# Performance work log

Measured on AMD Instinct MI355X. Metric: run time of the kernel, lower is better.

## Reference

```python
import jax, jax.numpy as jnp
import numpy as np

N, D, H = 8192, 256, 128
KEEP_RATIO = 0.5
TEMP = 1.0
COS_EPS = 1e-4  # torch CosineSimilarity eps
NEG = -9e15


def setup_inputs() -> dict:
    key = jax.random.key(0)
    k1, k2, k3, k4 = jax.random.split(key, 4)
    features = jax.random.normal(k1, (N, D), dtype=jnp.float32)
    adj = jax.random.randint(k2, (N, N), 0, 2, dtype=jnp.int32)
    # module init: Linear weights ~ N(0, 0.001)
    Wq = jax.random.normal(k3, (H, D), dtype=jnp.float32) * 0.001
    Wk = jax.random.normal(k4, (H, D), dtype=jnp.float32) * 0.001
    return {"features": features, "adj": adj, "Wq": Wq, "Wk": Wk}


def _cos_normalize(x):
    # torch cosine: x / max(||x||, eps)
    n = jnp.linalg.norm(x, axis=-1, keepdims=True)
    return x / jnp.maximum(n, COS_EPS)


def reference(features, adj, Wq, Wk):
    # projections [N, H]
    Qn = _cos_normalize(features @ Wq.T)
    Kn = _cos_normalize(features @ Wk.T)
    # raw_att[i, j] = cos(Wq f_j, Wk f_i)  -> [N, N]
    raw_att = Kn @ Qn.T
    att = jnp.where(adj > 0, raw_att, NEG) * TEMP
    att = jax.nn.softmax(att, axis=1)
    prop_fea = att @ features  # [N, D]
    # nodes with no neighbors keep their own features
    adj_mask = (jnp.sum(adj, axis=1) > 0).astype(features.dtype)[:, None]
    prop_fea = adj_mask * prop_fea + (1.0 - adj_mask) * features
    # gate=None branch: fixed keep_ratio mixing
    return (1.0 - KEEP_RATIO) * prop_fea + KEEP_RATIO * features
```

## Files before the change

### kernel.cpp

```cpp
#include <hip/hip_runtime.h>
#include <stdint.h>
#include <stddef.h>

#define NN 8192
#define DD 256
#define HH 128

typedef short bf16x8  __attribute__((ext_vector_type(8)));
typedef float f32x4   __attribute__((ext_vector_type(4)));
typedef float f32x16  __attribute__((ext_vector_type(16)));
typedef int   i32x4   __attribute__((ext_vector_type(4)));

static __device__ __forceinline__ short f2bf(float x){
  unsigned u = __float_as_uint(x);
  u = (u + 0x7FFFu + ((u >> 16) & 1u)) >> 16;
  return (short)(unsigned short)u;
}
static __device__ __forceinline__ bf16x8 cvt8(const float* p){
  f32x4 a = *(const f32x4*)p;
  f32x4 b = *(const f32x4*)(p + 4);
  bf16x8 o;
  o[0]=f2bf(a[0]); o[1]=f2bf(a[1]); o[2]=f2bf(a[2]); o[3]=f2bf(a[3]);
  o[4]=f2bf(b[0]); o[5]=f2bf(b[1]); o[6]=f2bf(b[2]); o[7]=f2bf(b[3]);
  return o;
}
static __device__ __forceinline__ bf16x8 ld16(const void* p){
  i32x4 v = *(const i32x4*)p;
  return __builtin_bit_cast(bf16x8, v);
}

__global__ __launch_bounds__(256) void k_ftfrag(const float* __restrict__ f,
                                                unsigned short* __restrict__ ftf){
  int t = threadIdx.x;
  int fr = blockIdx.x * 4 + (t >> 6);
  int l  = t & 63;
  int jt = fr >> 3, dt = fr & 7;
  int j = jt * 16 + (l >> 5) * 8, d = dt * 32 + (l & 31);
  bf16x8 o;
  #pragma unroll
  for (int e = 0; e < 8; ++e) o[e] = f2bf(f[(size_t)(j + e) * DD + d]);
  *(bf16x8*)(ftf + (size_t)fr * 512 + l * 8) = o;
}

__global__ __launch_bounds__(256) void k_proj(const float* __restrict__ f,
                                              const float* __restrict__ Wq,
                                              const float* __restrict__ Wk,
                                              unsigned short* __restrict__ Qnf,
                                              unsigned short* __restrict__ Kn){
  int t = threadIdx.x, wave = t >> 6, l = t & 63;
  int i0 = blockIdx.x * 64 + wave * 16;
  int lr = l & 15, lk = l >> 4;
  bf16x8 ka[8];
  #pragma unroll
  for (int ks = 0; ks < 8; ++ks)
    ka[ks] = cvt8(f + (size_t)(i0 + lr) * DD + ks * 32 + lk * 8);
  for (int pj = 0; pj < 2; ++pj){
    const float* W = pj ? Wk : Wq;
    f32x4 acc[8];
    #pragma unroll
    for (int n = 0; n < 8; ++n) acc[n] = (f32x4){0.f,0.f,0.f,0.f};
    for (int ks = 0; ks < 8; ++ks)
      #pragma unroll
      for (int n = 0; n < 8; ++n){
        bf16x8 bb = cvt8(W + (size_t)(n * 16 + lr) * DD + ks * 32 + lk * 8);
        acc[n] = __builtin_amdgcn_mfma_f32_16x16x32_bf16(ka[ks], bb, acc[n], 0, 0, 0);
      }
    #pragma unroll
    for (int r = 0; r < 4; ++r){
      float n2 = 0.f;
      #pragma unroll
      for (int n = 0; n < 8; ++n){ float v = acc[n][r]; n2 += v * v; }
      n2 += __shfl_xor(n2, 1); n2 += __shfl_xor(n2, 2);
      n2 += __shfl_xor(n2, 4); n2 += __shfl_xor(n2, 8);
      float s = 1.f / fmaxf(sqrtf(n2), 1e-4f);
      int row = i0 + lk * 4 + r;
      #pragma unroll
      for (int n = 0; n < 8; ++n){
        short v = f2bf(acc[n][r] * s);
        if (pj){
          Kn[(size_t)row * HH + n * 16 + lr] = (unsigned short)v;
        } else {
          size_t off = ((size_t)(row >> 5) * 8 + n) * 512
                     + ((row & 31) + 32 * (lr >> 3)) * 8 + (lr & 7);
          Qnf[off] = (unsigned short)v;
        }
      }
    }
  }
}

__global__ __launch_bounds__(256, 2) void k_attn(
      const int* __restrict__ adj,
      const unsigned short* __restrict__ Qnf, const unsigned short* __restrict__ Kn,
      const unsigned short* __restrict__ ftf,
      float* __restrict__ num_p, float* __restrict__ den_p){
  __shared__ __attribute__((aligned(16))) char p_lds[8192];
  __shared__ __attribute__((aligned(16))) int adj_lds[2][64][64];
  int t = threadIdx.x, wave = t >> 6, l = t & 63;
  int lc = l & 31, h = l >> 5;
  int ig = wave >> 1, jg = wave & 1, wq = wave;
  int ib = blockIdx.x >> 2, js = blockIdx.x & 3;
  int i0 = ib * 64;
  int jbase = js * 2048;

  bf16x8 kb[8];
  { const unsigned short* kp = Kn + (size_t)(i0 + ig * 32 + lc) * HH + h * 8;
    #pragma unroll
    for (int hs = 0; hs < 8; ++hs) kb[hs] = ld16(kp + hs * 16); }

  f32x16 pv00, pv01, pv10, pv11;
  #pragma unroll
  for (int e = 0; e < 16; ++e){ pv00[e]=0.f; pv01[e]=0.f; pv10[e]=0.f; pv11[e]=0.f; }
  float dacc[16];
  #pragma unroll
  for (int r = 0; r < 16; ++r) dacc[r] = 0.f;

  int arow = wave * 16 + (l >> 4);
  int acol = (l & 15) * 4;

  #pragma unroll
  for (int k4 = 0; k4 < 4; ++k4){
    i32x4 v = __builtin_nontemporal_load(
        (const i32x4*)(adj + (size_t)(i0 + arow + k4 * 4) * NN + jbase + acol));
    *(i32x4*)&adj_lds[0][arow + k4 * 4][acol] = v;
  }
  __syncthreads();

  for (int s = 0; s < 32; ++s){
    int j0 = jbase + s * 64;
    int cur = s & 1, nxt = cur ^ 1;

    bf16x8 qv[8];
    { const unsigned short* qb = Qnf + ((size_t)((j0 + jg * 32) >> 5) * 8) * 512 + (size_t)l * 8;
      #pragma unroll
      for (int hs = 0; hs < 8; ++hs) qv[hs] = ld16(qb + hs * 512); }

    i32x4 av[4];
    if (s < 31){
      #pragma unroll
      for (int k4 = 0; k4 < 4; ++k4)
        av[k4] = __builtin_nontemporal_load(
            (const i32x4*)(adj + (size_t)(i0 + arow + k4 * 4) * NN + j0 + 64 + acol));
    }

    bf16x8 bv[8];
    { const unsigned short* fb = ftf + ((size_t)(j0 >> 4) * 8 + wq * 2) * 512 + (size_t)l * 8;
      #pragma unroll
      for (int ks = 0; ks < 4; ++ks){
        bv[ks * 2]     = ld16(fb + ks * 4096);
        bv[ks * 2 + 1] = ld16(fb + ks * 4096 + 512); } }

    f32x16 st;
    #pragma unroll
    for (int e = 0; e < 16; ++e) st[e] = 0.f;
    #pragma unroll
    for (int hs = 0; hs < 8; ++hs)
      st = __builtin_amdgcn_mfma_f32_32x32x16_bf16(kb[hs], qv[hs], st, 0, 0, 0);

    #pragma unroll
    for (int r = 0; r < 16; ++r){
      int row = ig * 32 + (r & 3) + 8 * (r >> 2) + 4 * h;
      int a = adj_lds[cur][row][jg * 32 + lc];
      float wv = (a > 0) ? __expf(st[r]) : 0.f;
      dacc[r] += wv;
      int byo = row * 128 + (((jg * 32 + lc) * 2) ^ ((row & 7) << 4));
      *(unsigned short*)(p_lds + byo) = (unsigned short)f2bf(wv);
    }
    __syncthreads();

    if (s < 31){
      #pragma unroll
      for (int k4 = 0; k4 < 4; ++k4)
        *(i32x4*)&adj_lds[nxt][arow + k4 * 4][acol] = av[k4];
    }

    #pragma unroll
    for (int ks = 0; ks < 4; ++ks){
      int ko = (ks * 32 + h * 16) ^ ((lc & 7) << 4);
      bf16x8 pa0 = ld16(p_lds + lc * 128 + ko);
      bf16x8 pa1 = ld16(p_lds + (32 + lc) * 128 + ko);
      pv00 = __builtin_amdgcn_mfma_f32_32x32x16_bf16(pa0, bv[ks*2],   pv00, 0,0,0);
      pv01 = __builtin_amdgcn_mfma_f32_32x32x16_bf16(pa0, bv[ks*2+1], pv01, 0,0,0);
      pv10 = __builtin_amdgcn_mfma_f32_32x32x16_bf16(pa1, bv[ks*2],   pv10, 0,0,0);
      pv11 = __builtin_amdgcn_mfma_f32_32x32x16_bf16(pa1, bv[ks*2+1], pv11, 0,0,0);
    }
    __syncthreads();
  }

  #pragma unroll
  for (int r = 0; r < 16; ++r){
    float v = dacc[r];
    v += __shfl_xor(v, 1); v += __shfl_xor(v, 2); v += __shfl_xor(v, 4);
    v += __shfl_xor(v, 8); v += __shfl_xor(v, 16);
    if (lc == 0){
      int i = i0 + ig * 32 + (r & 3) + 8 * (r >> 2) + 4 * h;
      den_p[(size_t)(js * 2 + jg) * NN + i] = v;
    }
  }
  float* np = num_p + (size_t)js * NN * DD;
  #pragma unroll
  for (int r = 0; r < 16; ++r){
    int i = i0 + (r & 3) + 8 * (r >> 2) + 4 * h;
    int d = wq * 64 + lc;
    np[(size_t)i * DD + d]             = pv00[r];
    np[(size_t)i * DD + d + 32]        = pv01[r];
    np[(size_t)(i + 32) * DD + d]      = pv10[r];
    np[(size_t)(i + 32) * DD + d + 32] = pv11[r];
  }
}

__global__ __launch_bounds__(256) void k_final(const float* __restrict__ num_p,
                                               const float* __restrict__ den_p,
                                               const float* __restrict__ f,
                                               float* __restrict__ out){
  int gid = blockIdx.x * 256 + threadIdx.x;
  int i = gid >> 6;
  f32x4 nv = (f32x4){0.f,0.f,0.f,0.f};
  float dv = 0.f;
  #pragma unroll
  for (int s = 0; s < 4; ++s)
    nv += *(const f32x4*)(num_p + (size_t)s * NN * DD + (size_t)gid * 4);
  #pragma unroll
  for (int s = 0; s < 8; ++s)
    dv += den_p[(size_t)s * NN + i];
  f32x4 fv = *(const f32x4*)(f + (size_t)gid * 4);
  f32x4 o;
  if (dv > 0.f){
    float inv = 0.5f / dv;
    o = nv * inv + fv * 0.5f;
  } else {
    o = fv;
  }
  *(f32x4*)(out + (size_t)gid * 4) = o;
}

extern "C" void kernel_launch(void* const* d_in, const int* in_sizes, int n_in,
                              void* d_out, int out_size, void* d_ws, size_t ws_size,
                              hipStream_t stream){
  (void)in_sizes; (void)n_in; (void)out_size;
  const float* feat = (const float*)d_in[0];
  const int*   adj  = (const int*)d_in[1];
  const float* Wq   = (const float*)d_in[2];
  const float* Wk   = (const float*)d_in[3];
  float* out = (float*)d_out;
  char* ws = (char*)d_ws;
  unsigned short* Qnf  = (unsigned short*)(ws);
  unsigned short* Kn   = (unsigned short*)(ws + (2u << 20));
  unsigned short* ftf  = (unsigned short*)(ws + (4u << 20));
  float*          num_p = (float*)(ws + (8u << 20));
  float*          den_p = (float*)(ws + (40u << 20));
  if (ws_size < (40u << 20) + 262144u) return;

  k_ftfrag<<<1024, 256, 0, stream>>>(feat, ftf);
  k_proj<<<128, 256, 0, stream>>>(feat, Wq, Wk, Qnf, Kn);
  k_attn<<<512, 256, 0, stream>>>(adj, Qnf, Kn, ftf, num_p, den_p);
  k_final<<<2048, 256, 0, stream>>>(num_p, den_p, feat, out);
}
```

Before: 219.9 us.

## Pack adjacency into bitmask in a pre-pass and read bits in attention kernel

Adds a k_pack kernel that turns the int32 adjacency matrix into a 1-bit-per-entry mask using wave ballots. The attention kernel then reads one 32-bit word per row per 32-column group instead of staging int32 adjacency tiles through double-buffered LDS. This removes the LDS adjacency buffer and its staging stores, and shrinks the adjacency traffic inside the attention kernel. The full 256 MB adjacency is still read once in the extra pre-pass launch, and the attention kernel now does many small uncoalesced word loads per lane.

Result: slower. 289.1 us (+31.5%).

```diff
diff --git a/kernel.cpp b/kernel.cpp
--- a/kernel.cpp
+++ b/kernel.cpp
@@ -89,13 +89,27 @@
   }
 }
 
+__global__ __launch_bounds__(256) void k_pack(const int* __restrict__ adj,
+                                              unsigned* __restrict__ bits){
+  int wave = threadIdx.x >> 6, l = threadIdx.x & 63;
+  int gw = blockIdx.x * 4 + wave;
+  int row = gw >> 3, chunk = gw & 7;
+  const int* ap = adj + (size_t)row * NN + chunk * 1024 + l;
+  unsigned long long* bp = (unsigned long long*)(bits + (size_t)row * 256 + chunk * 32);
+  #pragma unroll
+  for (int it = 0; it < 16; ++it){
+    int v = ap[it * 64];
+    unsigned long long m = __ballot(v > 0);
+    if (l == 0) bp[it] = m;
+  }
+}
+
 __global__ __launch_bounds__(256, 2) void k_attn(
-      const int* __restrict__ adj,
+      const unsigned* __restrict__ bits,
       const unsigned short* __restrict__ Qnf, const unsigned short* __restrict__ Kn,
       const unsigned short* __restrict__ ftf,
       float* __restrict__ num_p, float* __restrict__ den_p){
   __shared__ __attribute__((aligned(16))) char p_lds[8192];
-  __shared__ __attribute__((aligned(16))) int adj_lds[2][64][64];
   int t = threadIdx.x, wave = t >> 6, l = t & 63;
   int lc = l & 31, h = l >> 5;
   int ig = wave >> 1, jg = wave & 1, wq = wave;
@@ -115,32 +129,20 @@
   #pragma unroll
   for (int r = 0; r < 16; ++r) dacc[r] = 0.f;
 
-  int arow = wave * 16 + (l >> 4);
-  int acol = (l & 15) * 4;
-
-  #pragma unroll
-  for (int k4 = 0; k4 < 4; ++k4){
-    i32x4 v = __builtin_nontemporal_load(
-        (const i32x4*)(adj + (size_t)(i0 + arow + k4 * 4) * NN + jbase + acol));
-    *(i32x4*)&adj_lds[0][arow + k4 * 4][acol] = v;
-  }
-  __syncthreads();
-
   for (int s = 0; s < 32; ++s){
     int j0 = jbase + s * 64;
-    int cur = s & 1, nxt = cur ^ 1;
 
     bf16x8 qv[8];
     { const unsigned short* qb = Qnf + ((size_t)((j0 + jg * 32) >> 5) * 8) * 512 + (size_t)l * 8;
       #pragma unroll
       for (int hs = 0; hs < 8; ++hs) qv[hs] = ld16(qb + hs * 512); }
 
-    i32x4 av[4];
-    if (s < 31){
-      #pragma unroll
-      for (int k4 = 0; k4 < 4; ++k4)
-        av[k4] = __builtin_nontemporal_load(
-            (const i32x4*)(adj + (size_t)(i0 + arow + k4 * 4) * NN + j0 + 64 + acol));
+    int w0 = (j0 >> 5) + jg;
+    unsigned mw[16];
+    #pragma unroll
+    for (int r = 0; r < 16; ++r){
+      int row = i0 + ig * 32 + (r & 3) + 8 * (r >> 2) + 4 * h;
+      mw[r] = bits[(size_t)row * 256 + w0];
     }
 
     bf16x8 bv[8];
@@ -160,19 +162,12 @@
     #pragma unroll
     for (int r = 0; r < 16; ++r){
       int row = ig * 32 + (r & 3) + 8 * (r >> 2) + 4 * h;
-      int a = adj_lds[cur][row][jg * 32 + lc];
-      float wv = (a > 0) ? __expf(st[r]) : 0.f;
+      float wv = ((mw[r] >> lc) & 1u) ? __expf(st[r]) : 0.f;
       dacc[r] += wv;
       int byo = row * 128 + (((jg * 32 + lc) * 2) ^ ((row & 7) << 4));
       *(unsigned short*)(p_lds + byo) = (unsigned short)f2bf(wv);
     }
     __syncthreads();
-
-    if (s < 31){
-      #pragma unroll
-      for (int k4 = 0; k4 < 4; ++k4)
-        *(i32x4*)&adj_lds[nxt][arow + k4 * 4][acol] = av[k4];
-    }
 
     #pragma unroll
     for (int ks = 0; ks < 4; ++ks){
@@ -247,12 +242,14 @@
   unsigned short* Qnf  = (unsigned short*)(ws);
   unsigned short* Kn   = (unsigned short*)(ws + (2u << 20));
   unsigned short* ftf  = (unsigned short*)(ws + (4u << 20));
-  float*          num_p = (float*)(ws + (8u << 20));
-  float*          den_p = (float*)(ws + (40u << 20));
-  if (ws_size < (40u << 20) + 262144u) return;
-
+  unsigned*       bits = (unsigned*)(ws + (8u << 20));
+  float*          num_p = (float*)(ws + (16u << 20));
+  float*          den_p = (float*)(ws + (48u << 20));
+  if (ws_size < (48u << 20) + 262144u) return;
+
+  k_pack<<<16384, 256, 0, stream>>>(adj, bits);
   k_ftfrag<<<1024, 256, 0, stream>>>(feat, ftf);
   k_proj<<<128, 256, 0, stream>>>(feat, Wq, Wk, Qnf, Kn);
-  k_attn<<<512, 256, 0, stream>>>(adj, Qnf, Kn, ftf, num_p, den_p);
+  k_attn<<<512, 256, 0, stream>>>(bits, Qnf, Kn, ftf, num_p, den_p);
   k_final<<<2048, 256, 0, stream>>>(num_p, den_p, feat, out);
 }
```
